# Kernel optimization log

Hardware: AMD Instinct MI355X
Metric: run time of the kernel (lower is better)

Reference implementation:

```python
import jax, jax.numpy as jnp
import numpy as np

N = 50000      # nodes
E = 800000     # edges
H = 64         # num_hidden
NUM_LAYERS = 4 # -> NUM_LAYERS-1 shared-weight processor steps
EPS = 1e-12


def _mlp3(x, w1, b1, w2, b2, w3, b3):
    h = jax.nn.relu(x @ w1 + b1)
    h = jax.nn.relu(h @ w2 + b2)
    return h @ w3 + b3


def setup_inputs() -> dict:
    key = jax.random.key(0)
    ks = jax.random.split(key, 32)

    def gl(k, shape):
        fan_in = shape[0]
        return (jax.random.normal(k, shape, jnp.float32) / np.sqrt(fan_in)).astype(jnp.float32)

    inp = {
        "X_curr": jax.random.normal(ks[0], (N, 6), jnp.float32),
        "y_prev": jax.random.normal(ks[1], (N,), jnp.float32),
        "edge": jax.random.randint(ks[2], (2, E), 0, N, dtype=jnp.int64),
        # edge net: Linear(9,H) ReLU Linear(H,H) ReLU Linear(H,3)
        "ew1": gl(ks[3], (9, H)), "eb1": jnp.zeros((H,), jnp.float32),
        "ew2": gl(ks[4], (H, H)), "eb2": jnp.zeros((H,), jnp.float32),
        "ew3": gl(ks[5], (H, 3)), "eb3": jnp.zeros((3,), jnp.float32),
        # node net: Linear(5,H) ReLU Linear(H,H) ReLU Linear(H,1)
        "nw1": gl(ks[6], (5, H)), "nb1": jnp.zeros((H,), jnp.float32),
        "nw2": gl(ks[7], (H, H)), "nb2": jnp.zeros((H,), jnp.float32),
        "nw3": gl(ks[8], (H, 1)), "nb3": jnp.zeros((1,), jnp.float32),
        # decoder: Linear(5,H) ReLU Linear(H,H) ReLU Linear(H,H) ReLU Linear(H,1)
        "dw1": gl(ks[9], (5, H)),  "db1": jnp.zeros((H,), jnp.float32),
        "dw2": gl(ks[10], (H, H)), "db2": jnp.zeros((H,), jnp.float32),
        "dw3": gl(ks[11], (H, H)), "db3": jnp.zeros((H,), jnp.float32),
        "dw4": gl(ks[12], (H, 1)), "db4": jnp.zeros((1,), jnp.float32),
        "mode": 0,
    }
    return inp


def reference(X_curr, y_prev, edge,
              ew1, eb1, ew2, eb2, ew3, eb3,
              nw1, nb1, nw2, nb2, nw3, nb3,
              dw1, db1, dw2, db2, dw3, db3, dw4, db4,
              mode):
    src, dst = edge[0], edge[1]
    n = X_curr.shape[0]

    # x_in: [N,5] = (pos x,y,z, feature col 4, y_prev)
    x_in = jnp.concatenate([X_curr[:, jnp.array([0, 1, 2, 4])], y_prev[:, None]], axis=-1)

    # initial edge_attr = (f_dest - f_src) * disp  -> [E,3]
    disp0 = x_in[dst, :3] - x_in[src, :3]
    f_r = x_in[dst, 4] - x_in[src, 4]
    edge_attr = f_r[:, None] * disp0

    cnt = jax.ops.segment_sum(jnp.ones((edge.shape[1], 1), x_in.dtype), dst, num_segments=n)
    denom = jnp.maximum(cnt, 1.0)

    for _ in range(NUM_LAYERS - 1):  # shared weights across processors
        xs = x_in[src]
        xd = x_in[dst]
        disp = xd[:, :3] - xs[:, :3]
        norm = jnp.sqrt(jnp.sum(disp * disp, axis=-1, keepdims=True) + EPS)
        net_in = jnp.concatenate([disp, norm, edge_attr, xs[:, 4:5], xd[:, 4:5]], axis=-1)  # [E,9]
        edge_attr = edge_attr + _mlp3(net_in, ew1, eb1, ew2, eb2, ew3, eb3)

        # scatter-mean of edge_attr at destination nodes
        aggr = jax.ops.segment_sum(edge_attr, dst, num_segments=n) / denom  # [N,3]
        node_in = jnp.concatenate([x_in[:, 3:5], aggr], axis=-1)            # [N,5]
        delta = _mlp3(node_in, nw1, nb1, nw2, nb2, nw3, nb3)[:, 0]
        x_in = jnp.concatenate([x_in[:, :4], (x_in[:, 4] + delta)[:, None]], axis=-1)

    # decoder
    h = jax.nn.relu(x_in @ dw1 + db1)
    h = jax.nn.relu(h @ dw2 + db2)
    h = jax.nn.relu(h @ dw3 + db3)
    x_out = h @ dw4 + db4  # [N,1]
    return y_prev + x_out[:, 0]
```

## Files before the change

### kernel.cpp

```cpp
#include <hip/hip_runtime.h>
#include <math.h>

#define N_NODES 50000
#define N_EDGES 800000
#define EPS 1e-12f
#define SCAN_NB 196
#define MAXB 6144

typedef __attribute__((ext_vector_type(8))) short bf16x8;
typedef __attribute__((ext_vector_type(4))) float f32x4;

__device__ inline unsigned pk_bf16(float a, float b) {
    unsigned ua = __float_as_uint(a), ub = __float_as_uint(b);
    ua = (ua + 0x7FFFu + ((ua >> 16) & 1u)) >> 16;
    ub = (ub + 0x7FFFu + ((ub >> 16) & 1u)) >> 16;
    return ua | (ub << 16);
}

#define W1OFF 0
#define W2OFF 4096
#define W3OFF 13312
#define RS 144
#define EB1 15616
#define EB2 15872
#define EB3 16128
#define EIMG_B 16192
#define DW1OFF 0
#define DW2OFF 4096
#define DW3OFF 13312
#define DW4OFF 22528
#define DB1 24832
#define DB2 25088
#define DB3 25344
#define DB4 25600
#define DIMG_B 25664

__global__ void k_node_init(const float* __restrict__ X, const float* __restrict__ yp,
                            float4* __restrict__ px4, float* __restrict__ f) {
    int n = blockIdx.x * blockDim.x + threadIdx.x;
    if (n < N_NODES) {
        px4[n] = make_float4(X[n * 6 + 0], X[n * 6 + 1], X[n * 6 + 2], X[n * 6 + 4]);
        f[n] = yp[n];
    }
}

__global__ __launch_bounds__(256) void k_prep(
    const float* __restrict__ ew1, const float* __restrict__ ew2,
    const float* __restrict__ ew3, const float* __restrict__ eb1,
    const float* __restrict__ eb2, const float* __restrict__ eb3,
    const float* __restrict__ nw1, const float* __restrict__ nw2,
    const float* __restrict__ nw3, const float* __restrict__ nb1,
    const float* __restrict__ nb2, const float* __restrict__ nb3,
    const float* __restrict__ dw1, const float* __restrict__ dw2,
    const float* __restrict__ dw3, const float* __restrict__ dw4,
    const float* __restrict__ db1, const float* __restrict__ db2,
    const float* __restrict__ db3, const float* __restrict__ db4,
    char* __restrict__ eimg, char* __restrict__ nimg, char* __restrict__ dimg) {
    const int t = threadIdx.x;
    const int n = t & 63, kg = t >> 6;
    const int n3 = t & 15, kg3 = t >> 4;
    if (blockIdx.x == 0) {
        unsigned pk[4];
#pragma unroll
        for (int i = 0; i < 4; i++) {
            int k0 = kg * 8 + i * 2;
            float v0 = (k0 < 9) ? ew1[k0 * 64 + n] : 0.f;
            float v1 = (k0 + 1 < 9) ? ew1[(k0 + 1) * 64 + n] : 0.f;
            pk[i] = pk_bf16(v0, v1);
        }
        *(uint4*)(eimg + W1OFF + n * 64 + kg * 16) = make_uint4(pk[0], pk[1], pk[2], pk[3]);
        unsigned pk2[8];
#pragma unroll
        for (int i = 0; i < 8; i++) {
            int k0 = kg * 16 + i * 2;
            pk2[i] = pk_bf16(ew2[k0 * 64 + n], ew2[(k0 + 1) * 64 + n]);
        }
        *(uint4*)(eimg + W2OFF + n * RS + kg * 32) = make_uint4(pk2[0], pk2[1], pk2[2], pk2[3]);
        *(uint4*)(eimg + W2OFF + n * RS + kg * 32 + 16) = make_uint4(pk2[4], pk2[5], pk2[6], pk2[7]);
        unsigned pk3[2];
#pragma unroll
        for (int i = 0; i < 2; i++) {
            int k0 = kg3 * 4 + i * 2;
            float v0 = (n3 < 3) ? ew3[k0 * 3 + n3] : 0.f;
            float v1 = (n3 < 3) ? ew3[(k0 + 1) * 3 + n3] : 0.f;
            pk3[i] = pk_bf16(v0, v1);
        }
        *(uint2*)(eimg + W3OFF + n3 * RS + kg3 * 8) = make_uint2(pk3[0], pk3[1]);
        if (t < 64) {
            ((float*)(eimg + EB1))[t] = eb1[t];
            ((float*)(eimg + EB2))[t] = eb2[t];
        }
        if (t < 16) ((float*)(eimg + EB3))[t] = (t < 3) ? eb3[t] : 0.f;
    } else if (blockIdx.x == 1) {
        unsigned pk[4];
#pragma unroll
        for (int i = 0; i < 4; i++) {
            int k0 = kg * 8 + i * 2;
            float v0 = (k0 < 5) ? nw1[k0 * 64 + n] : 0.f;
            float v1 = (k0 + 1 < 5) ? nw1[(k0 + 1) * 64 + n] : 0.f;
            pk[i] = pk_bf16(v0, v1);
        }
        *(uint4*)(nimg + W1OFF + n * 64 + kg * 16) = make_uint4(pk[0], pk[1], pk[2], pk[3]);
        unsigned pk2[8];
#pragma unroll
        for (int i = 0; i < 8; i++) {
            int k0 = kg * 16 + i * 2;
            pk2[i] = pk_bf16(nw2[k0 * 64 + n], nw2[(k0 + 1) * 64 + n]);
        }
        *(uint4*)(nimg + W2OFF + n * RS + kg * 32) = make_uint4(pk2[0], pk2[1], pk2[2], pk2[3]);
        *(uint4*)(nimg + W2OFF + n * RS + kg * 32 + 16) = make_uint4(pk2[4], pk2[5], pk2[6], pk2[7]);
        unsigned pk3[2];
#pragma unroll
        for (int i = 0; i < 2; i++) {
            int k0 = kg3 * 4 + i * 2;
            float v0 = (n3 == 0) ? nw3[k0] : 0.f;
            float v1 = (n3 == 0) ? nw3[k0 + 1] : 0.f;
            pk3[i] = pk_bf16(v0, v1);
        }
        *(uint2*)(nimg + W3OFF + n3 * RS + kg3 * 8) = make_uint2(pk3[0], pk3[1]);
        if (t < 64) {
            ((float*)(nimg + EB1))[t] = nb1[t];
            ((float*)(nimg + EB2))[t] = nb2[t];
        }
        if (t < 16) ((float*)(nimg + EB3))[t] = (t == 0) ? nb3[0] : 0.f;
    } else {
        unsigned pk[4];
#pragma unroll
        for (int i = 0; i < 4; i++) {
            int k0 = kg * 8 + i * 2;
            float v0 = (k0 < 5) ? dw1[k0 * 64 + n] : 0.f;
            float v1 = (k0 + 1 < 5) ? dw1[(k0 + 1) * 64 + n] : 0.f;
            pk[i] = pk_bf16(v0, v1);
        }
        *(uint4*)(dimg + DW1OFF + n * 64 + kg * 16) = make_uint4(pk[0], pk[1], pk[2], pk[3]);
        unsigned pk2[8], pk3b[8];
#pragma unroll
        for (int i = 0; i < 8; i++) {
            int k0 = kg * 16 + i * 2;
            pk2[i] = pk_bf16(dw2[k0 * 64 + n], dw2[(k0 + 1) * 64 + n]);
            pk3b[i] = pk_bf16(dw3[k0 * 64 + n], dw3[(k0 + 1) * 64 + n]);
        }
        *(uint4*)(dimg + DW2OFF + n * RS + kg * 32) = make_uint4(pk2[0], pk2[1], pk2[2], pk2[3]);
        *(uint4*)(dimg + DW2OFF + n * RS + kg * 32 + 16) = make_uint4(pk2[4], pk2[5], pk2[6], pk2[7]);
        *(uint4*)(dimg + DW3OFF + n * RS + kg * 32) = make_uint4(pk3b[0], pk3b[1], pk3b[2], pk3b[3]);
        *(uint4*)(dimg + DW3OFF + n * RS + kg * 32 + 16) = make_uint4(pk3b[4], pk3b[5], pk3b[6], pk3b[7]);
        unsigned pk4[2];
#pragma unroll
        for (int i = 0; i < 2; i++) {
            int k0 = kg3 * 4 + i * 2;
            float v0 = (n3 == 0) ? dw4[k0] : 0.f;
            float v1 = (n3 == 0) ? dw4[k0 + 1] : 0.f;
            pk4[i] = pk_bf16(v0, v1);
        }
        *(uint2*)(dimg + DW4OFF + n3 * RS + kg3 * 8) = make_uint2(pk4[0], pk4[1]);
        if (t < 64) {
            ((float*)(dimg + DB1))[t] = db1[t];
            ((float*)(dimg + DB2))[t] = db2[t];
            ((float*)(dimg + DB3))[t] = db3[t];
        }
        if (t < 16) ((float*)(dimg + DB4))[t] = (t == 0) ? db4[0] : 0.f;
    }
}

__global__ __launch_bounds__(256) void k_bucket(const int* __restrict__ edge,
                                                int* __restrict__ btail,
                                                int2* __restrict__ staging) {
    __shared__ int hist[256], loff[256], gbase[256], fill[256];
    __shared__ int2 ebL[2048];
    __shared__ unsigned short bktL[2048];
    const int t = threadIdx.x;
    const int base = blockIdx.x * 2048;
    const int cnt = min(2048, N_EDGES - base);
    hist[t] = 0; fill[t] = 0;
    __syncthreads();

    int2 my[8]; int mb[8];
#pragma unroll
    for (int j = 0; j < 8; j++) {
        int i = base + t + j * 256;
        if (i < N_EDGES) {
            int s = edge[i], d = edge[N_EDGES + i];
            my[j] = make_int2(s, d);
            mb[j] = d >> 8;
            atomicAdd(&hist[mb[j]], 1);
        } else mb[j] = -1;
    }
    __syncthreads();
    int v = hist[t];
    loff[t] = v;
    __syncthreads();
    for (int off = 1; off < 256; off <<= 1) {
        int x = (t >= off) ? loff[t - off] : 0;
        __syncthreads();
        loff[t] += x;
        __syncthreads();
    }
    int ex = loff[t] - v;
    __syncthreads();
    loff[t] = ex;
    if (v > 0) gbase[t] = atomicAdd(&btail[t], v);
    __syncthreads();
#pragma unroll
    for (int j = 0; j < 8; j++) {
        if (mb[j] >= 0) {
            int lp = loff[mb[j]] + atomicAdd(&fill[mb[j]], 1);
            ebL[lp] = my[j];
            bktL[lp] = (unsigned short)mb[j];
        }
    }
    __syncthreads();
    for (int i = t; i < cnt; i += 256) {
        int b = bktL[i];
        int gp = gbase[b] + (i - loff[b]);
        if (gp < MAXB) staging[b * MAXB + gp] = ebL[i];
    }
}

__global__ void k_bscan(const int* __restrict__ btail, int* __restrict__ bbase) {
    __shared__ int s[256];
    int t = threadIdx.x;
    int v = (t < SCAN_NB) ? btail[t] : 0;
    s[t] = v;
    __syncthreads();
    for (int off = 1; off < 256; off <<= 1) {
        int x = (t >= off) ? s[t - off] : 0;
        __syncthreads();
        s[t] += x;
        __syncthreads();
    }
    if (t < SCAN_NB) bbase[t] = s[t] - v;
}

__global__ __launch_bounds__(256) void k_bsort(const int2* __restrict__ staging,
                                               const int* __restrict__ btail,
                                               const int* __restrict__ bbase,
                                               int2* __restrict__ sd,
                                               int* __restrict__ rowptr) {
    __shared__ int hist[256], excl[256], fill[256], sbuf[256];
    __shared__ int2 ebL[MAXB];
    const int b = blockIdx.x, t = threadIdx.x;
    const int size = min(btail[b], MAXB);
    const int gb = bbase[b];
    for (int i = t; i < size; i += 256) ebL[i] = staging[b * MAXB + i];
    hist[t] = 0; fill[t] = 0;
    __syncthreads();
    for (int i = t; i < size; i += 256) atomicAdd(&hist[ebL[i].y & 255], 1);
    __syncthreads();
    int v = hist[t];
    sbuf[t] = v;
    __syncthreads();
    for (int off = 1; off < 256; off <<= 1) {
        int x = (t >= off) ? sbuf[t - off] : 0;
        __syncthreads();
        sbuf[t] += x;
        __syncthreads();
    }
    int ex = sbuf[t] - v;
    excl[t] = ex;
    int n = (b << 8) + t;
    if (n < N_NODES) rowptr[n] = gb + ex;
    if (b == SCAN_NB - 1 && t == 0) rowptr[N_NODES] = N_EDGES;
    __syncthreads();
    for (int i = t; i < size; i += 256) {
        int2 v2 = ebL[i];
        int ld = v2.y & 255;
        int pos = excl[ld] + atomicAdd(&fill[ld], 1);
        sd[gb + pos] = v2;
    }
}

__global__ void k_edge_init(const int2* __restrict__ sd,
                            const float4* __restrict__ px4,
                            const float* __restrict__ yp,
                            float4* __restrict__ dnrm, float4* __restrict__ ea) {
    int e = blockIdx.x * blockDim.x + threadIdx.x;
    if (e < N_EDGES) {
        int2 SD = sd[e];
        float4 ps = px4[SD.x], pd = px4[SD.y];
        float dx = pd.x - ps.x, dy = pd.y - ps.y, dz = pd.z - ps.z;
        float nrm = sqrtf(dx * dx + dy * dy + dz * dz + EPS);
        dnrm[e] = make_float4(dx, dy, dz, nrm);
        float fr = yp[SD.y] - yp[SD.x];
        ea[e] = make_float4(fr * dx, fr * dy, fr * dz, 0.f);
    }
}

__global__ __launch_bounds__(256, 2) void k_edge_mlp(
    const int2* __restrict__ sd, const float4* __restrict__ dnrm,
    float4* __restrict__ ea, const float* __restrict__ f,
    const char* __restrict__ eimg) {
    __shared__ __align__(16) char smem[EIMG_B + 4 * 64 * RS];
    const int t = threadIdx.x;
    const int lane = t & 63, wave = t >> 6;
    const int c = lane & 15, q = lane >> 4;

    for (int i = t; i < EIMG_B / 16; i += 256)
        ((uint4*)smem)[i] = ((const uint4*)eimg)[i];

    char* mybuf = smem + EIMG_B + wave * (64 * RS);
    const int e = blockIdx.x * 256 + t;
    int2 SD = sd[e];
    float4 DN = dnrm[e];
    float4 EA = ea[e];
    float fs = f[SD.x], fd = f[SD.y];
    {
        char* row = mybuf + lane * RS;
        *(uint4*)(row) = make_uint4(pk_bf16(DN.x, DN.y), pk_bf16(DN.z, DN.w),
                                    pk_bf16(EA.x, EA.y), pk_bf16(EA.z, fs));
        *(uint4*)(row + 16) = make_uint4(pk_bf16(fd, 0.f), 0u, 0u, 0u);
        *(uint4*)(row + 32) = make_uint4(0u, 0u, 0u, 0u);
        *(uint4*)(row + 48) = make_uint4(0u, 0u, 0u, 0u);
    }
    __syncthreads();

    bf16x8 Wa1[4], Wa2[8], Wa3[2];
#pragma unroll
    for (int mt = 0; mt < 4; mt++)
        Wa1[mt] = *(bf16x8*)(smem + W1OFF + (mt * 16 + c) * 64 + q * 16);
#pragma unroll
    for (int mt = 0; mt < 4; mt++)
#pragma unroll
        for (int ks = 0; ks < 2; ks++)
            Wa2[mt * 2 + ks] =
                *(bf16x8*)(smem + W2OFF + (mt * 16 + c) * RS + ks * 64 + q * 16);
#pragma unroll
    for (int ks = 0; ks < 2; ks++)
        Wa3[ks] = *(bf16x8*)(smem + W3OFF + c * RS + ks * 64 + q * 16);
    float4 b1v[4], b2v[4], b3v;
#pragma unroll
    for (int mt = 0; mt < 4; mt++) {
        b1v[mt] = *(const float4*)(smem + EB1 + (mt * 16 + q * 4) * 4);
        b2v[mt] = *(const float4*)(smem + EB2 + (mt * 16 + q * 4) * 4);
    }
    b3v = *(const float4*)(smem + EB3 + q * 16);

#pragma unroll
    for (int nt = 0; nt < 4; nt++) {
        char* rowb = mybuf + (nt * 16 + c) * RS;
        bf16x8 Eb = *(bf16x8*)(rowb + q * 16);
        f32x4 a1[4];
#pragma unroll
        for (int mt = 0; mt < 4; mt++) {
            a1[mt] = (f32x4){b1v[mt].x, b1v[mt].y, b1v[mt].z, b1v[mt].w};
            a1[mt] = __builtin_amdgcn_mfma_f32_16x16x32_bf16(Wa1[mt], Eb, a1[mt], 0, 0, 0);
        }
#pragma unroll
        for (int mt = 0; mt < 4; mt++)
            *(uint2*)(rowb + mt * 32 + q * 8) = make_uint2(
                pk_bf16(fmaxf(a1[mt][0], 0.f), fmaxf(a1[mt][1], 0.f)),
                pk_bf16(fmaxf(a1[mt][2], 0.f), fmaxf(a1[mt][3], 0.f)));
        bf16x8 H0 = *(bf16x8*)(rowb + q * 16);
        bf16x8 H1 = *(bf16x8*)(rowb + 64 + q * 16);
        f32x4 a2[4];
#pragma unroll
        for (int mt = 0; mt < 4; mt++) {
            a2[mt] = (f32x4){b2v[mt].x, b2v[mt].y, b2v[mt].z, b2v[mt].w};
            a2[mt] = __builtin_amdgcn_mfma_f32_16x16x32_bf16(Wa2[mt * 2 + 0], H0, a2[mt], 0, 0, 0);
            a2[mt] = __builtin_amdgcn_mfma_f32_16x16x32_bf16(Wa2[mt * 2 + 1], H1, a2[mt], 0, 0, 0);
        }
#pragma unroll
        for (int mt = 0; mt < 4; mt++)
            *(uint2*)(rowb + mt * 32 + q * 8) = make_uint2(
                pk_bf16(fmaxf(a2[mt][0], 0.f), fmaxf(a2[mt][1], 0.f)),
                pk_bf16(fmaxf(a2[mt][2], 0.f), fmaxf(a2[mt][3], 0.f)));
        bf16x8 G0 = *(bf16x8*)(rowb + q * 16);
        bf16x8 G1 = *(bf16x8*)(rowb + 64 + q * 16);
        f32x4 a3 = (f32x4){b3v.x, b3v.y, b3v.z, b3v.w};
        a3 = __builtin_amdgcn_mfma_f32_16x16x32_bf16(Wa3[0], G0, a3, 0, 0, 0);
        a3 = __builtin_amdgcn_mfma_f32_16x16x32_bf16(Wa3[1], G1, a3, 0, 0, 0);
        if (q == 0)
            *(float4*)(rowb + 128) = make_float4(a3[0], a3[1], a3[2], a3[3]);
    }

    float4 o = *(float4*)(mybuf + lane * RS + 128);
    ea[e] = make_float4(EA.x + o.x, EA.y + o.y, EA.z + o.z, 0.f);
}

__global__ __launch_bounds__(256, 2) void k_node_mlp(
    const float4* __restrict__ px4, float* __restrict__ f,
    const float4* __restrict__ ea, const int* __restrict__ rowptr,
    const char* __restrict__ nimg) {
    __shared__ __align__(16) char smem[EIMG_B + 4 * 64 * RS];
    const int t = threadIdx.x;
    const int lane = t & 63, wave = t >> 6;
    const int c = lane & 15, q = lane >> 4;

    for (int i = t; i < EIMG_B / 16; i += 256)
        ((uint4*)smem)[i] = ((const uint4*)nimg)[i];

    char* mybuf = smem + EIMG_B + wave * (64 * RS);
    const int idx = blockIdx.x * 256 + t;
    const int n = (idx < N_NODES) ? idx : (N_NODES - 1);

    int b0 = rowptr[n], b1 = rowptr[n + 1];
    float a0 = 0.f, a1s = 0.f, a2s = 0.f;
    for (int p = b0; p < b1; p++) {
        float4 v = ea[p];
        a0 += v.x; a1s += v.y; a2s += v.z;
    }
    float inv = 1.0f / fmaxf((float)(b1 - b0), 1.0f);
    float4 P = px4[n];
    float fn = f[n];
    {
        char* row = mybuf + lane * RS;
        *(uint4*)(row) = make_uint4(pk_bf16(P.w, fn), pk_bf16(a0 * inv, a1s * inv),
                                    pk_bf16(a2s * inv, 0.f), 0u);
        *(uint4*)(row + 16) = make_uint4(0u, 0u, 0u, 0u);
        *(uint4*)(row + 32) = make_uint4(0u, 0u, 0u, 0u);
        *(uint4*)(row + 48) = make_uint4(0u, 0u, 0u, 0u);
    }
    __syncthreads();

    bf16x8 Wa1[4], Wa2[8], Wa3[2];
#pragma unroll
    for (int mt = 0; mt < 4; mt++)
        Wa1[mt] = *(bf16x8*)(smem + W1OFF + (mt * 16 + c) * 64 + q * 16);
#pragma unroll
    for (int mt = 0; mt < 4; mt++)
#pragma unroll
        for (int ks = 0; ks < 2; ks++)
            Wa2[mt * 2 + ks] =
                *(bf16x8*)(smem + W2OFF + (mt * 16 + c) * RS + ks * 64 + q * 16);
#pragma unroll
    for (int ks = 0; ks < 2; ks++)
        Wa3[ks] = *(bf16x8*)(smem + W3OFF + c * RS + ks * 64 + q * 16);
    float4 b1v[4], b2v[4], b3v;
#pragma unroll
    for (int mt = 0; mt < 4; mt++) {
        b1v[mt] = *(const float4*)(smem + EB1 + (mt * 16 + q * 4) * 4);
        b2v[mt] = *(const float4*)(smem + EB2 + (mt * 16 + q * 4) * 4);
    }
    b3v = *(const float4*)(smem + EB3 + q * 16);

#pragma unroll
    for (int nt = 0; nt < 4; nt++) {
        char* rowb = mybuf + (nt * 16 + c) * RS;
        bf16x8 Eb = *(bf16x8*)(rowb + q * 16);
        f32x4 a1v[4];
#pragma unroll
        for (int mt = 0; mt < 4; mt++) {
            a1v[mt] = (f32x4){b1v[mt].x, b1v[mt].y, b1v[mt].z, b1v[mt].w};
            a1v[mt] = __builtin_amdgcn_mfma_f32_16x16x32_bf16(Wa1[mt], Eb, a1v[mt], 0, 0, 0);
        }
#pragma unroll
        for (int mt = 0; mt < 4; mt++)
            *(uint2*)(rowb + mt * 32 + q * 8) = make_uint2(
                pk_bf16(fmaxf(a1v[mt][0], 0.f), fmaxf(a1v[mt][1], 0.f)),
                pk_bf16(fmaxf(a1v[mt][2], 0.f), fmaxf(a1v[mt][3], 0.f)));
        bf16x8 H0 = *(bf16x8*)(rowb + q * 16);
        bf16x8 H1 = *(bf16x8*)(rowb + 64 + q * 16);
        f32x4 a2v[4];
#pragma unroll
        for (int mt = 0; mt < 4; mt++) {
            a2v[mt] = (f32x4){b2v[mt].x, b2v[mt].y, b2v[mt].z, b2v[mt].w};
            a2v[mt] = __builtin_amdgcn_mfma_f32_16x16x32_bf16(Wa2[mt * 2 + 0], H0, a2v[mt], 0, 0, 0);
            a2v[mt] = __builtin_amdgcn_mfma_f32_16x16x32_bf16(Wa2[mt * 2 + 1], H1, a2v[mt], 0, 0, 0);
        }
#pragma unroll
        for (int mt = 0; mt < 4; mt++)
            *(uint2*)(rowb + mt * 32 + q * 8) = make_uint2(
                pk_bf16(fmaxf(a2v[mt][0], 0.f), fmaxf(a2v[mt][1], 0.f)),
                pk_bf16(fmaxf(a2v[mt][2], 0.f), fmaxf(a2v[mt][3], 0.f)));
        bf16x8 G0 = *(bf16x8*)(rowb + q * 16);
        bf16x8 G1 = *(bf16x8*)(rowb + 64 + q * 16);
        f32x4 a3 = (f32x4){b3v.x, b3v.y, b3v.z, b3v.w};
        a3 = __builtin_amdgcn_mfma_f32_16x16x32_bf16(Wa3[0], G0, a3, 0, 0, 0);
        a3 = __builtin_amdgcn_mfma_f32_16x16x32_bf16(Wa3[1], G1, a3, 0, 0, 0);
        if (q == 0) *(float*)(rowb + 128) = a3[0];
    }

    float o = *(float*)(mybuf + lane * RS + 128);
    if (idx < N_NODES) f[n] = fn + o;
}

__global__ __launch_bounds__(256, 2) void k_decoder(
    const float4* __restrict__ px4, const float* __restrict__ f,
    const float* __restrict__ yp, const char* __restrict__ dimg,
    float* __restrict__ out) {
    __shared__ __align__(16) char smem[DIMG_B + 4 * 64 * RS];
    const int t = threadIdx.x;
    const int lane = t & 63, wave = t >> 6;
    const int c = lane & 15, q = lane >> 4;

    for (int i = t; i < DIMG_B / 16; i += 256)
        ((uint4*)smem)[i] = ((const uint4*)dimg)[i];

    char* mybuf = smem + DIMG_B + wave * (64 * RS);
    const int idx = blockIdx.x * 256 + t;
    const int n = (idx < N_NODES) ? idx : (N_NODES - 1);
    float4 P = px4[n];
    float fn = f[n];
    {
        char* row = mybuf + lane * RS;
        *(uint4*)(row) = make_uint4(pk_bf16(P.x, P.y), pk_bf16(P.z, P.w),
                                    pk_bf16(fn, 0.f), 0u);
        *(uint4*)(row + 16) = make_uint4(0u, 0u, 0u, 0u);
        *(uint4*)(row + 32) = make_uint4(0u, 0u, 0u, 0u);
        *(uint4*)(row + 48) = make_uint4(0u, 0u, 0u, 0u);
    }
    __syncthreads();

    bf16x8 Wa1[4], Wa2[8], Wa3[8], Wa4[2];
#pragma unroll
    for (int mt = 0; mt < 4; mt++)
        Wa1[mt] = *(bf16x8*)(smem + DW1OFF + (mt * 16 + c) * 64 + q * 16);
#pragma unroll
    for (int mt = 0; mt < 4; mt++)
#pragma unroll
        for (int ks = 0; ks < 2; ks++) {
            Wa2[mt * 2 + ks] =
                *(bf16x8*)(smem + DW2OFF + (mt * 16 + c) * RS + ks * 64 + q * 16);
            Wa3[mt * 2 + ks] =
                *(bf16x8*)(smem + DW3OFF + (mt * 16 + c) * RS + ks * 64 + q * 16);
        }
#pragma unroll
    for (int ks = 0; ks < 2; ks++)
        Wa4[ks] = *(bf16x8*)(smem + DW4OFF + c * RS + ks * 64 + q * 16);
    float4 b1v[4], b2v[4], b3v[4], b4v;
#pragma unroll
    for (int mt = 0; mt < 4; mt++) {
        b1v[mt] = *(const float4*)(smem + DB1 + (mt * 16 + q * 4) * 4);
        b2v[mt] = *(const float4*)(smem + DB2 + (mt * 16 + q * 4) * 4);
        b3v[mt] = *(const float4*)(smem + DB3 + (mt * 16 + q * 4) * 4);
    }
    b4v = *(const float4*)(smem + DB4 + q * 16);

#pragma unroll
    for (int nt = 0; nt < 4; nt++) {
        char* rowb = mybuf + (nt * 16 + c) * RS;
        bf16x8 Eb = *(bf16x8*)(rowb + q * 16);
        f32x4 a1v[4];
#pragma unroll
        for (int mt = 0; mt < 4; mt++) {
            a1v[mt] = (f32x4){b1v[mt].x, b1v[mt].y, b1v[mt].z, b1v[mt].w};
            a1v[mt] = __builtin_amdgcn_mfma_f32_16x16x32_bf16(Wa1[mt], Eb, a1v[mt], 0, 0, 0);
        }
#pragma unroll
        for (int mt = 0; mt < 4; mt++)
            *(uint2*)(rowb + mt * 32 + q * 8) = make_uint2(
                pk_bf16(fmaxf(a1v[mt][0], 0.f), fmaxf(a1v[mt][1], 0.f)),
                pk_bf16(fmaxf(a1v[mt][2], 0.f), fmaxf(a1v[mt][3], 0.f)));
        bf16x8 H0 = *(bf16x8*)(rowb + q * 16);
        bf16x8 H1 = *(bf16x8*)(rowb + 64 + q * 16);
        f32x4 a2v[4];
#pragma unroll
        for (int mt = 0; mt < 4; mt++) {
            a2v[mt] = (f32x4){b2v[mt].x, b2v[mt].y, b2v[mt].z, b2v[mt].w};
            a2v[mt] = __builtin_amdgcn_mfma_f32_16x16x32_bf16(Wa2[mt * 2 + 0], H0, a2v[mt], 0, 0, 0);
            a2v[mt] = __builtin_amdgcn_mfma_f32_16x16x32_bf16(Wa2[mt * 2 + 1], H1, a2v[mt], 0, 0, 0);
        }
#pragma unroll
        for (int mt = 0; mt < 4; mt++)
            *(uint2*)(rowb + mt * 32 + q * 8) = make_uint2(
                pk_bf16(fmaxf(a2v[mt][0], 0.f), fmaxf(a2v[mt][1], 0.f)),
                pk_bf16(fmaxf(a2v[mt][2], 0.f), fmaxf(a2v[mt][3], 0.f)));
        bf16x8 G0 = *(bf16x8*)(rowb + q * 16);
        bf16x8 G1 = *(bf16x8*)(rowb + 64 + q * 16);
        f32x4 a3v[4];
#pragma unroll
        for (int mt = 0; mt < 4; mt++) {
            a3v[mt] = (f32x4){b3v[mt].x, b3v[mt].y, b3v[mt].z, b3v[mt].w};
            a3v[mt] = __builtin_amdgcn_mfma_f32_16x16x32_bf16(Wa3[mt * 2 + 0], G0, a3v[mt], 0, 0, 0);
            a3v[mt] = __builtin_amdgcn_mfma_f32_16x16x32_bf16(Wa3[mt * 2 + 1], G1, a3v[mt], 0, 0, 0);
        }
#pragma unroll
        for (int mt = 0; mt < 4; mt++)
            *(uint2*)(rowb + mt * 32 + q * 8) = make_uint2(
                pk_bf16(fmaxf(a3v[mt][0], 0.f), fmaxf(a3v[mt][1], 0.f)),
                pk_bf16(fmaxf(a3v[mt][2], 0.f), fmaxf(a3v[mt][3], 0.f)));
        bf16x8 F0 = *(bf16x8*)(rowb + q * 16);
        bf16x8 F1 = *(bf16x8*)(rowb + 64 + q * 16);
        f32x4 a4 = (f32x4){b4v.x, b4v.y, b4v.z, b4v.w};
        a4 = __builtin_amdgcn_mfma_f32_16x16x32_bf16(Wa4[0], F0, a4, 0, 0, 0);
        a4 = __builtin_amdgcn_mfma_f32_16x16x32_bf16(Wa4[1], F1, a4, 0, 0, 0);
        if (q == 0) *(float*)(rowb + 128) = a4[0];
    }

    float o = *(float*)(mybuf + lane * RS + 128);
    if (idx < N_NODES) out[n] = yp[n] + o;
}

extern "C" void kernel_launch(void* const* d_in, const int* in_sizes, int n_in,
                              void* d_out, int out_size, void* d_ws, size_t ws_size,
                              hipStream_t stream) {
    const float* X    = (const float*)d_in[0];
    const float* yp   = (const float*)d_in[1];
    const int*   edge = (const int*)d_in[2];
    const float *ew1 = (const float*)d_in[3],  *eb1 = (const float*)d_in[4];
    const float *ew2 = (const float*)d_in[5],  *eb2 = (const float*)d_in[6];
    const float *ew3 = (const float*)d_in[7],  *eb3 = (const float*)d_in[8];
    const float *nw1 = (const float*)d_in[9],  *nb1 = (const float*)d_in[10];
    const float *nw2 = (const float*)d_in[11], *nb2 = (const float*)d_in[12];
    const float *nw3 = (const float*)d_in[13], *nb3 = (const float*)d_in[14];
    const float *dw1 = (const float*)d_in[15], *db1 = (const float*)d_in[16];
    const float *dw2 = (const float*)d_in[17], *db2 = (const float*)d_in[18];
    const float *dw3 = (const float*)d_in[19], *db3 = (const float*)d_in[20];
    const float *dw4 = (const float*)d_in[21], *db4 = (const float*)d_in[22];
    float* out = (float*)d_out;

    char* p = (char*)d_ws;
    auto carve = [&](size_t bytes) {
        char* r = p;
        p += (bytes + 255) & ~(size_t)255;
        return r;
    };
    int2*   sd     = (int2*)  carve(sizeof(int2)   * N_EDGES);
    float4* dnrm   = (float4*)carve(sizeof(float4) * N_EDGES);
    float4* ea     = (float4*)carve(sizeof(float4) * N_EDGES);
    float4* px4    = (float4*)carve(sizeof(float4) * N_NODES);
    float*  f      = (float*) carve(sizeof(float)  * N_NODES);
    int*    rowptr = (int*)   carve(sizeof(int)    * (N_NODES + 1));
    int*    btail  = (int*)   carve(sizeof(int)    * 256);
    int*    bbase  = (int*)   carve(sizeof(int)    * 256);
    char*   eimg   = (char*)  carve(EIMG_B);
    char*   nimg   = (char*)  carve(EIMG_B);
    char*   dimg   = (char*)  carve(DIMG_B);
    int2*   staging = (int2*)dnrm;

    const int nb_n = SCAN_NB;
    const int nb_e = (N_EDGES + 255) / 256;
    const int nb_b = (N_EDGES + 2047) / 2048;

    hipMemsetAsync(btail, 0, sizeof(int) * 256, stream);
    k_node_init<<<nb_n, 256, 0, stream>>>(X, yp, px4, f);
    k_prep<<<3, 256, 0, stream>>>(ew1, ew2, ew3, eb1, eb2, eb3,
                                  nw1, nw2, nw3, nb1, nb2, nb3,
                                  dw1, dw2, dw3, dw4, db1, db2, db3, db4,
                                  eimg, nimg, dimg);
    k_bucket<<<nb_b, 256, 0, stream>>>(edge, btail, staging);
    k_bscan<<<1, 256, 0, stream>>>(btail, bbase);
    k_bsort<<<SCAN_NB, 256, 0, stream>>>(staging, btail, bbase, sd, rowptr);
    k_edge_init<<<nb_e, 256, 0, stream>>>(sd, px4, yp, dnrm, ea);

    for (int it = 0; it < 3; ++it) {
        k_edge_mlp<<<nb_e, 256, 0, stream>>>(sd, dnrm, ea, f, eimg);
        k_node_mlp<<<nb_n, 256, 0, stream>>>(px4, f, ea, rowptr, nimg);
    }
    k_decoder<<<nb_n, 256, 0, stream>>>(px4, f, yp, dimg, out);
}
```

Baseline: 280.6 us.

## Fuse init kernels, fold bucket scan and edge init into sort

Merges node init and weight prep into one kernel. Each sort block now redoes the 196-entry bucket-offset scan itself, which removes the separate scan kernel. The sort scatter loop also computes the displacement, norm and initial edge attributes directly, which removes the edge-init kernel and its reread of the sorted edge list. Staging gets its own workspace buffer instead of aliasing dnrm, since dnrm is now written during the sort. This cuts three launches but makes the dnrm/ea writes scattered, and the sort blocks do extra redundant scan work.

```diff
diff --git a/kernel.cpp b/kernel.cpp
--- a/kernel.cpp
+++ b/kernel.cpp
@@ -35,16 +35,9 @@
 #define DB4 25600
 #define DIMG_B 25664
 
-__global__ void k_node_init(const float* __restrict__ X, const float* __restrict__ yp,
-                            float4* __restrict__ px4, float* __restrict__ f) {
-    int n = blockIdx.x * blockDim.x + threadIdx.x;
-    if (n < N_NODES) {
-        px4[n] = make_float4(X[n * 6 + 0], X[n * 6 + 1], X[n * 6 + 2], X[n * 6 + 4]);
-        f[n] = yp[n];
-    }
-}
-
-__global__ __launch_bounds__(256) void k_prep(
+__global__ __launch_bounds__(256) void k_init(
+    const float* __restrict__ X, const float* __restrict__ yp,
+    float4* __restrict__ px4, float* __restrict__ f,
     const float* __restrict__ ew1, const float* __restrict__ ew2,
     const float* __restrict__ ew3, const float* __restrict__ eb1,
     const float* __restrict__ eb2, const float* __restrict__ eb3,
@@ -57,6 +50,14 @@
     const float* __restrict__ db3, const float* __restrict__ db4,
     char* __restrict__ eimg, char* __restrict__ nimg, char* __restrict__ dimg) {
     const int t = threadIdx.x;
+    if (blockIdx.x >= 3) {
+        int n = (blockIdx.x - 3) * 256 + t;
+        if (n < N_NODES) {
+            px4[n] = make_float4(X[n * 6 + 0], X[n * 6 + 1], X[n * 6 + 2], X[n * 6 + 4]);
+            f[n] = yp[n];
+        }
+        return;
+    }
     const int n = t & 63, kg = t >> 6;
     const int n3 = t & 15, kg3 = t >> 4;
     if (blockIdx.x == 0) {
@@ -216,38 +217,20 @@
     }
 }
 
-__global__ void k_bscan(const int* __restrict__ btail, int* __restrict__ bbase) {
-    __shared__ int s[256];
-    int t = threadIdx.x;
-    int v = (t < SCAN_NB) ? btail[t] : 0;
-    s[t] = v;
-    __syncthreads();
-    for (int off = 1; off < 256; off <<= 1) {
-        int x = (t >= off) ? s[t - off] : 0;
-        __syncthreads();
-        s[t] += x;
-        __syncthreads();
-    }
-    if (t < SCAN_NB) bbase[t] = s[t] - v;
-}
-
 __global__ __launch_bounds__(256) void k_bsort(const int2* __restrict__ staging,
                                                const int* __restrict__ btail,
-                                               const int* __restrict__ bbase,
+                                               const float4* __restrict__ px4,
+                                               const float* __restrict__ yp,
                                                int2* __restrict__ sd,
+                                               float4* __restrict__ dnrm,
+                                               float4* __restrict__ ea,
                                                int* __restrict__ rowptr) {
     __shared__ int hist[256], excl[256], fill[256], sbuf[256];
     __shared__ int2 ebL[MAXB];
     const int b = blockIdx.x, t = threadIdx.x;
-    const int size = min(btail[b], MAXB);
-    const int gb = bbase[b];
-    for (int i = t; i < size; i += 256) ebL[i] = staging[b * MAXB + i];
-    hist[t] = 0; fill[t] = 0;
-    __syncthreads();
-    for (int i = t; i < size; i += 256) atomicAdd(&hist[ebL[i].y & 255], 1);
-    __syncthreads();
-    int v = hist[t];
-    sbuf[t] = v;
+
+    int bv = (t < SCAN_NB) ? btail[t] : 0;
+    sbuf[t] = bv;
     __syncthreads();
     for (int off = 1; off < 256; off <<= 1) {
         int x = (t >= off) ? sbuf[t - off] : 0;
@@ -255,6 +238,23 @@
         sbuf[t] += x;
         __syncthreads();
     }
+    const int gb = (b == 0) ? 0 : sbuf[b - 1];
+    const int size = min(btail[b], MAXB);
+
+    for (int i = t; i < size; i += 256) ebL[i] = staging[b * MAXB + i];
+    hist[t] = 0; fill[t] = 0;
+    __syncthreads();
+    for (int i = t; i < size; i += 256) atomicAdd(&hist[ebL[i].y & 255], 1);
+    __syncthreads();
+    int v = hist[t];
+    sbuf[t] = v;
+    __syncthreads();
+    for (int off = 1; off < 256; off <<= 1) {
+        int x = (t >= off) ? sbuf[t - off] : 0;
+        __syncthreads();
+        sbuf[t] += x;
+        __syncthreads();
+    }
     int ex = sbuf[t] - v;
     excl[t] = ex;
     int n = (b << 8) + t;
@@ -265,23 +265,14 @@
         int2 v2 = ebL[i];
         int ld = v2.y & 255;
         int pos = excl[ld] + atomicAdd(&fill[ld], 1);
-        sd[gb + pos] = v2;
-    }
-}
-
-__global__ void k_edge_init(const int2* __restrict__ sd,
-                            const float4* __restrict__ px4,
-                            const float* __restrict__ yp,
-                            float4* __restrict__ dnrm, float4* __restrict__ ea) {
-    int e = blockIdx.x * blockDim.x + threadIdx.x;
-    if (e < N_EDGES) {
-        int2 SD = sd[e];
-        float4 ps = px4[SD.x], pd = px4[SD.y];
+        int gp = gb + pos;
+        sd[gp] = v2;
+        float4 ps = px4[v2.x], pd = px4[v2.y];
         float dx = pd.x - ps.x, dy = pd.y - ps.y, dz = pd.z - ps.z;
         float nrm = sqrtf(dx * dx + dy * dy + dz * dz + EPS);
-        dnrm[e] = make_float4(dx, dy, dz, nrm);
-        float fr = yp[SD.y] - yp[SD.x];
-        ea[e] = make_float4(fr * dx, fr * dy, fr * dz, 0.f);
+        dnrm[gp] = make_float4(dx, dy, dz, nrm);
+        float fr = yp[v2.y] - yp[v2.x];
+        ea[gp] = make_float4(fr * dx, fr * dy, fr * dz, 0.f);
     }
 }
 
@@ -604,33 +595,31 @@
         p += (bytes + 255) & ~(size_t)255;
         return r;
     };
-    int2*   sd     = (int2*)  carve(sizeof(int2)   * N_EDGES);
-    float4* dnrm   = (float4*)carve(sizeof(float4) * N_EDGES);
-    float4* ea     = (float4*)carve(sizeof(float4) * N_EDGES);
-    float4* px4    = (float4*)carve(sizeof(float4) * N_NODES);
-    float*  f      = (float*) carve(sizeof(float)  * N_NODES);
-    int*    rowptr = (int*)   carve(sizeof(int)    * (N_NODES + 1));
-    int*    btail  = (int*)   carve(sizeof(int)    * 256);
-    int*    bbase  = (int*)   carve(sizeof(int)    * 256);
-    char*   eimg   = (char*)  carve(EIMG_B);
-    char*   nimg   = (char*)  carve(EIMG_B);
-    char*   dimg   = (char*)  carve(DIMG_B);
-    int2*   staging = (int2*)dnrm;
+    int2*   sd      = (int2*)  carve(sizeof(int2)   * N_EDGES);
+    float4* dnrm    = (float4*)carve(sizeof(float4) * N_EDGES);
+    float4* ea      = (float4*)carve(sizeof(float4) * N_EDGES);
+    int2*   staging = (int2*)  carve(sizeof(int2)   * SCAN_NB * MAXB);
+    float4* px4     = (float4*)carve(sizeof(float4) * N_NODES);
+    float*  f       = (float*) carve(sizeof(float)  * N_NODES);
+    int*    rowptr  = (int*)   carve(sizeof(int)    * (N_NODES + 1));
+    int*    btail   = (int*)   carve(sizeof(int)    * 256);
+    char*   eimg    = (char*)  carve(EIMG_B);
+    char*   nimg    = (char*)  carve(EIMG_B);
+    char*   dimg    = (char*)  carve(DIMG_B);
 
     const int nb_n = SCAN_NB;
     const int nb_e = (N_EDGES + 255) / 256;
     const int nb_b = (N_EDGES + 2047) / 2048;
 
     hipMemsetAsync(btail, 0, sizeof(int) * 256, stream);
-    k_node_init<<<nb_n, 256, 0, stream>>>(X, yp, px4, f);
-    k_prep<<<3, 256, 0, stream>>>(ew1, ew2, ew3, eb1, eb2, eb3,
-                                  nw1, nw2, nw3, nb1, nb2, nb3,
-                                  dw1, dw2, dw3, dw4, db1, db2, db3, db4,
-                                  eimg, nimg, dimg);
+    k_init<<<3 + nb_n, 256, 0, stream>>>(X, yp, px4, f,
+                                         ew1, ew2, ew3, eb1, eb2, eb3,
+                                         nw1, nw2, nw3, nb1, nb2, nb3,
+                                         dw1, dw2, dw3, dw4, db1, db2, db3, db4,
+                                         eimg, nimg, dimg);
     k_bucket<<<nb_b, 256, 0, stream>>>(edge, btail, staging);
-    k_bscan<<<1, 256, 0, stream>>>(btail, bbase);
-    k_bsort<<<SCAN_NB, 256, 0, stream>>>(staging, btail, bbase, sd, rowptr);
-    k_edge_init<<<nb_e, 256, 0, stream>>>(sd, px4, yp, dnrm, ea);
+    k_bsort<<<nb_n, 256, 0, stream>>>(staging, btail, px4, yp,
+                                      sd, dnrm, ea, rowptr);
 
     for (int it = 0; it < 3; ++it) {
         k_edge_mlp<<<nb_e, 256, 0, stream>>>(sd, dnrm, ea, f, eimg);
```

New measurement: 291.3 us. 3.8% more time.
